# Kernel optimization log

Hardware: AMD Instinct MI355X
Metric: run time of the kernel (lower is better)

## Reference

```python
import jax, jax.numpy as jnp
import numpy as np

N, E, ELG, B = 50000, 400000, 1600000, 2000
F, ED, T = 64, 16, 6
SND = 6 * F  # LinearBlock hidden


def segment_softmax(x, seg, num_segments):
    m = jax.ops.segment_max(x, seg, num_segments=num_segments)
    e = jnp.exp(x - m[seg])
    s = jax.ops.segment_sum(e, seg, num_segments=num_segments)
    return e / (s[seg] + 1e-16)


def setup_inputs() -> dict:
    key = jax.random.key(0)
    ks = jax.random.split(key, 32)
    d = {}
    d['x'] = jax.random.normal(ks[0], (N, F), jnp.float32)
    d['edge_attr'] = jax.random.normal(ks[1], (E, ED), jnp.float32)
    d['edge_index'] = jax.random.randint(ks[2], (2, E), 0, N, jnp.int32)
    d['line_graph_edge_index'] = jax.random.randint(ks[3], (2, ELG), 0, E, jnp.int32)
    d['edge_index_batch'] = jnp.sort(jax.random.randint(ks[4], (E,), 0, B, jnp.int32))
    g = lambda k, shp, fi: jax.random.normal(k, shp, jnp.float32) * (1.0 / np.sqrt(fi))
    d['W_u'] = g(ks[5], (F, F), F)
    d['W_v'] = g(ks[6], (F, F), F)
    d['W_e'] = g(ks[7], (F, ED), ED)
    # GraphConv(F, 1): lin_rel (bias) on aggregated msgs + lin_root (no bias)
    d['conv_w_rel'] = g(ks[8], (1, F), F)
    d['conv_b_rel'] = jnp.zeros((1,), jnp.float32)
    d['conv_w_root'] = g(ks[9], (1, F), F)
    glorot_a = np.sqrt(6.0 / (F + T))
    d['a'] = jax.random.uniform(ks[10], (1, F, T), jnp.float32, -glorot_a, glorot_a)
    d['W_gout'] = g(ks[11], (F, F), F)
    d['b_gout'] = jnp.zeros((F,), jnp.float32)
    d['a_bias'] = jnp.zeros((1, 1, T), jnp.float32)
    d['lb1_w'] = g(ks[12], (SND, F), F); d['lb1_b'] = jnp.zeros((SND,), jnp.float32)
    d['lb2_w'] = g(ks[13], (SND, SND), SND); d['lb2_b'] = jnp.zeros((SND,), jnp.float32)
    d['lb3_w'] = g(ks[14], (SND, SND), SND); d['lb3_b'] = jnp.zeros((SND,), jnp.float32)
    d['lb4_w'] = g(ks[15], (SND, SND), SND); d['lb4_b'] = jnp.zeros((SND,), jnp.float32)
    d['lb5_w'] = g(ks[16], (F, SND), SND); d['lb5_b'] = jnp.zeros((F,), jnp.float32)
    return d


def reference(x, edge_attr, edge_index, line_graph_edge_index, edge_index_batch,
              W_u, W_v, W_e, conv_w_rel, conv_b_rel, conv_w_root,
              a, W_gout, b_gout, a_bias,
              lb1_w, lb1_b, lb2_w, lb2_b, lb3_w, lb3_b, lb4_w, lb4_b, lb5_w, lb5_b):
    src, dst = edge_index[0], edge_index[1]
    lsrc, ldst = line_graph_edge_index[0], line_graph_edge_index[1]
    # initial directed-edge features
    edge_feat = (x @ W_u.T)[src] + (x @ W_v.T)[dst] + edge_attr @ W_e.T  # [E,F]
    edge_feat = edge_feat / 3.0
    out = edge_feat
    outs, gouts = [], []
    for _ in range(T):  # fixed small iteration count
        agg = jax.ops.segment_sum(out[lsrc], ldst, num_segments=E)  # line-graph scatter-add
        out = edge_feat + agg
        # GlobalAttentionPool: GraphConv(F,1) on line graph, segment softmax, add-pool
        conv_agg = jax.ops.segment_sum(out[lsrc], ldst, num_segments=E)
        x_conv = conv_agg @ conv_w_rel.T + conv_b_rel + out @ conv_w_root.T  # [E,1]
        sc = segment_softmax(x_conv, edge_index_batch, B)  # [E,1]
        g = jax.ops.segment_sum(out * sc, edge_index_batch, num_segments=B)  # [B,F]
        outs.append(out)
        gouts.append(jnp.tanh(g @ W_gout.T + b_gout))
    gout_all = jnp.stack(gouts, axis=-1)  # [B,F,T]
    out_all = jnp.stack(outs, axis=-1)    # [E,F,T]
    scores = (gout_all * a).sum(1, keepdims=True) + a_bias  # [B,1,T]
    scores = jax.nn.softmax(scores, axis=-1)
    scores_e = scores[edge_index_batch]  # == repeat_interleave by degree (sorted batch)
    out_w = (out_all * scores_e).sum(-1)  # [E,F]
    h = x + jax.ops.segment_sum(out_w, dst, num_segments=N)
    # LinearBlock (SA-DDI lineage)
    h = jax.nn.relu(h @ lb1_w.T + lb1_b)
    h = (jax.nn.relu(h @ lb2_w.T + lb2_b) @ lb3_w.T + lb3_b + h) / 2.0
    h = (h @ lb4_w.T + lb4_b + h) / 2.0
    return jax.nn.relu(h @ lb5_w.T + lb5_b)
```

## Files before the change

kernel.cpp:

```cpp
#include <hip/hip_runtime.h>
#include <hip/hip_fp16.h>

#define N_   50000
#define E_   400000
#define ELG_ 1600000
#define B_   2000
#define F_   64
#define ED_  16
#define T_   6
#define SND_ 384

typedef long long ll;
typedef _Float16 f16x8 __attribute__((ext_vector_type(8)));
typedef float f32x4 __attribute__((ext_vector_type(4)));

__device__ inline float ldc(const float* p, ll i) { return p[i]; }
__device__ inline float ldc(const __half* p, ll i) { return __half2float(p[i]); }
__device__ inline void st1(float* p, float v) { *p = v; }
__device__ inline void st1(__half* p, float v) { *p = __float2half(v); }

template <int FPL>
__device__ inline void ldN(const float* p, float (&o)[FPL]) {
#pragma unroll
    for (int c = 0; c < FPL; c += 4) {
        float4 v = *(const float4*)(p + c);
        o[c] = v.x; o[c + 1] = v.y; o[c + 2] = v.z; o[c + 3] = v.w;
    }
}
template <int FPL>
__device__ inline void ldN(const __half* p, float (&o)[FPL]) {
#pragma unroll
    for (int c = 0; c < FPL; c += 8) {
        float4 raw = *(const float4*)(p + c);
        const __half2* h = (const __half2*)&raw;
#pragma unroll
        for (int i = 0; i < 4; i++) {
            float2 f = __half22float2(h[i]);
            o[c + 2 * i] = f.x; o[c + 2 * i + 1] = f.y;
        }
    }
}
template <int FPL>
__device__ inline void stN(float* p, const float (&v)[FPL]) {
#pragma unroll
    for (int c = 0; c < FPL; c += 4)
        *(float4*)(p + c) = make_float4(v[c], v[c + 1], v[c + 2], v[c + 3]);
}
template <int FPL>
__device__ inline void stN(__half* p, const float (&v)[FPL]) {
#pragma unroll
    for (int c = 0; c < FPL; c += 8) {
        __half2 h[4];
#pragma unroll
        for (int i = 0; i < 4; i++) h[i] = __floats2half2_rn(v[c + 2 * i], v[c + 2 * i + 1]);
        *(float4*)(p + c) = *(const float4*)h;
    }
}

__global__ __launch_bounds__(256) void k_count(const int* __restrict__ ldst, int* __restrict__ cnt) {
    int i = blockIdx.x * 256 + threadIdx.x;
    if (i < ELG_) atomicAdd(&cnt[ldst[i]], 1);
}

__global__ __launch_bounds__(256) void k_scan1(const int* __restrict__ cnt, int* __restrict__ rowptr,
                                               int* __restrict__ bsum) {
    __shared__ int s[256];
    int tid = threadIdx.x;
    int i = blockIdx.x * 256 + tid;
    int v = (i < E_) ? cnt[i] : 0;
    s[tid] = v;
    __syncthreads();
    for (int off = 1; off < 256; off <<= 1) {
        int t = (tid >= off) ? s[tid - off] : 0;
        __syncthreads();
        s[tid] += t;
        __syncthreads();
    }
    if (i < E_) rowptr[i] = s[tid] - v;
    if (tid == 255) bsum[blockIdx.x] = s[255];
}

__global__ __launch_bounds__(256) void k_scan2(int* __restrict__ bsum, int nb) {
    __shared__ int s[256];
    __shared__ int carry_s;
    int tid = threadIdx.x;
    if (tid == 0) carry_s = 0;
    __syncthreads();
    for (int base = 0; base < nb; base += 256) {
        int i = base + tid;
        int v = (i < nb) ? bsum[i] : 0;
        s[tid] = v;
        __syncthreads();
        for (int off = 1; off < 256; off <<= 1) {
            int t = (tid >= off) ? s[tid - off] : 0;
            __syncthreads();
            s[tid] += t;
            __syncthreads();
        }
        int c = carry_s;
        if (i < nb) bsum[i] = s[tid] - v + c;
        __syncthreads();
        if (tid == 0) carry_s = c + s[255];
        __syncthreads();
    }
}

__global__ __launch_bounds__(256) void k_scan3(int* __restrict__ rowptr, const int* __restrict__ bsum) {
    int i = blockIdx.x * 256 + threadIdx.x;
    if (i < E_) rowptr[i] += bsum[i >> 8];
    if (i == 0) rowptr[E_] = ELG_;
}

__global__ __launch_bounds__(256) void k_fill(const int* __restrict__ lsrc, const int* __restrict__ ldst,
                                              const int* __restrict__ rowptr, int* __restrict__ cursor,
                                              int* __restrict__ csr) {
    int i = blockIdx.x * 256 + threadIdx.x;
    if (i < ELG_) {
        int d = ldst[i];
        int pos = atomicAdd(&cursor[d], 1);
        csr[rowptr[d] + pos] = lsrc[i];
    }
}

__global__ __launch_bounds__(256) void k_bptr(const int* __restrict__ eib, int* __restrict__ bptr) {
    int b = blockIdx.x * 256 + threadIdx.x;
    if (b > B_) return;
    int lo = 0, hi = E_;
    while (lo < hi) {
        int mid = (lo + hi) >> 1;
        if (eib[mid] < b) lo = mid + 1; else hi = mid;
    }
    bptr[b] = lo;
}

__global__ __launch_bounds__(256) void k_xuv(const float* __restrict__ x,
                                             const float* __restrict__ Wu, const float* __restrict__ Wv,
                                             float* __restrict__ xu, float* __restrict__ xv) {
    __shared__ float wus[64 * 65];
    __shared__ float wvs[64 * 65];
    __shared__ float xs[16][64];
    int tid = threadIdx.x;
    for (int i = tid; i < 4096; i += 256) {
        int f = i >> 6, k = i & 63;
        wus[k * 65 + f] = Wu[i];
        wvs[k * 65 + f] = Wv[i];
    }
    int r0 = blockIdx.x * 16;
    for (int i = tid; i < 16 * 64; i += 256) {
        int r = i >> 6, j = i & 63;
        int row = r0 + r;
        xs[r][j] = (row < N_) ? x[(ll)row * 64 + j] : 0.f;
    }
    __syncthreads();
    int j = tid & 63, lr0 = tid >> 6;
    float su[4] = {0, 0, 0, 0}, sv[4] = {0, 0, 0, 0};
    for (int k = 0; k < 64; k++) {
        float wu = wus[k * 65 + j];
        float wv = wvs[k * 65 + j];
#pragma unroll
        for (int r = 0; r < 4; r++) {
            float xr = xs[lr0 + r * 4][k];
            su[r] += xr * wu;
            sv[r] += xr * wv;
        }
    }
#pragma unroll
    for (int r = 0; r < 4; r++) {
        int row = r0 + lr0 + r * 4;
        if (row < N_) {
            xu[(ll)row * 64 + j] = su[r];
            xv[(ll)row * 64 + j] = sv[r];
        }
    }
}

template <typename ET>
__global__ __launch_bounds__(256) void k_ef(const float* __restrict__ xu, const float* __restrict__ xv,
                                            const float* __restrict__ ea, const float* __restrict__ We,
                                            const int* __restrict__ src, const int* __restrict__ dst,
                                            ET* __restrict__ ef) {
    __shared__ float wes[16 * 65];
    int tid = threadIdx.x;
    for (int i = tid; i < 1024; i += 256) {
        wes[(i & 15) * 65 + (i >> 4)] = We[i];
    }
    __syncthreads();
    int wid = tid >> 6, f = tid & 63;
    ll e0 = (ll)blockIdx.x * 16;
#pragma unroll
    for (int r = 0; r < 4; r++) {
        ll e = e0 + wid + r * 4;
        if (e >= E_) return;
        int s = src[e], d = dst[e];
        float v = xu[(ll)s * 64 + f] + xv[(ll)d * 64 + f];
#pragma unroll
        for (int k = 0; k < 16; k++) v += ea[e * 16 + k] * wes[k * 65 + f];
        st1(&ef[e * 64 + f], v * (1.0f / 3.0f));
    }
}

template <typename T, typename OT, bool WOUT, bool WXC, int ACC>
__global__ __launch_bounds__(256) void k_segv(
    const T* __restrict__ state, T* __restrict__ nxt, OT* __restrict__ outw,
    const float* __restrict__ xu, const float* __restrict__ xv,
    const float* __restrict__ ea, const float* __restrict__ We,
    const int* __restrict__ esrc, const int* __restrict__ edst,
    const int* __restrict__ rowptr, const int* __restrict__ csr,
    float* __restrict__ xc, const float* __restrict__ w_rel,
    const float* __restrict__ b_rel, const float* __restrict__ w_root,
    const float* __restrict__ scores, const int* __restrict__ eib, int tslot)
{
    constexpr int FPL = 16 / sizeof(T);
    constexpr int LPR = F_ / FPL;
    constexpr int RPB = 256 / LPR;
    constexpr bool EF = WOUT || (ACC > 0);
    __shared__ float wes[16 * 65];
    int tid = threadIdx.x;
    if (EF) {
        for (int i = tid; i < 1024; i += 256)
            wes[(i & 15) * 65 + (i >> 4)] = We[i];
        __syncthreads();
    }
    int sub = tid % LPR;
    int r   = tid / LPR;
    ll d = (ll)blockIdx.x * RPB + r;
    int f0 = sub * FPL;
    int p0 = rowptr[d], p1 = rowptr[d + 1];
    float acc[FPL], acc2[FPL];
#pragma unroll
    for (int j = 0; j < FPL; j++) { acc[j] = 0.f; acc2[j] = 0.f; }
    int p = p0;
    for (; p + 2 <= p1; p += 2) {
        int s0 = csr[p], s1 = csr[p + 1];
        float v0[FPL], v1[FPL];
        ldN<FPL>(&state[(ll)s0 * F_ + f0], v0);
        ldN<FPL>(&state[(ll)s1 * F_ + f0], v1);
#pragma unroll
        for (int j = 0; j < FPL; j++) { acc[j] += v0[j]; acc2[j] += v1[j]; }
    }
    if (p < p1) {
        int s0 = csr[p];
        float v0[FPL];
        ldN<FPL>(&state[(ll)s0 * F_ + f0], v0);
#pragma unroll
        for (int j = 0; j < FPL; j++) acc[j] += v0[j];
    }
#pragma unroll
    for (int j = 0; j < FPL; j++) acc[j] += acc2[j];
    if (EF) {
        int se = esrc[d], de = edst[d];
        float o[FPL], xuv[FPL], xvv[FPL];
        ldN<FPL>(&xu[(ll)se * 64 + f0], xuv);
        ldN<FPL>(&xv[(ll)de * 64 + f0], xvv);
#pragma unroll
        for (int j = 0; j < FPL; j++) o[j] = xuv[j] + xvv[j];
#pragma unroll
        for (int k = 0; k < 16; k++) {
            float eav = ea[d * 16 + k];
#pragma unroll
            for (int j = 0; j < FPL; j++) o[j] += eav * wes[k * 65 + f0 + j];
        }
#pragma unroll
        for (int j = 0; j < FPL; j++) o[j] = o[j] * (1.0f / 3.0f) + acc[j];
        if (WOUT) stN<FPL>(&nxt[(ll)d * F_ + f0], o);
        if (ACC > 0) {
            float w = scores[eib[d] * 6 + tslot];
            float ow[FPL];
            if (ACC == 2) ldN<FPL>(&outw[(ll)d * F_ + f0], ow);
            else {
#pragma unroll
                for (int j = 0; j < FPL; j++) ow[j] = 0.f;
            }
#pragma unroll
            for (int j = 0; j < FPL; j++) ow[j] += w * o[j];
            stN<FPL>(&outw[(ll)d * F_ + f0], ow);
        }
    }
    if (WXC) {
        float ov[FPL];
        ldN<FPL>(&state[(ll)d * F_ + f0], ov);
        float part = 0.f;
#pragma unroll
        for (int j = 0; j < FPL; j++)
            part += acc[j] * w_rel[f0 + j] + ov[j] * w_root[f0 + j];
#pragma unroll
        for (int off = LPR / 2; off; off >>= 1) part += __shfl_xor(part, off, 64);
        if (sub == 0) xc[d] = part + b_rel[0];
    }
}

template <typename ST>
__global__ __launch_bounds__(256) void k_pool(const float* __restrict__ xc, const ST* __restrict__ out_t,
                                              const int* __restrict__ bptr, const float* __restrict__ Wg,
                                              const float* __restrict__ bg, float* __restrict__ gouts,
                                              int tslot) {
    int b = blockIdx.x;
    int tid = threadIdx.x;
    int p0 = bptr[b], p1 = bptr[b + 1];
    __shared__ float red[256];
    __shared__ float gsh[64];
    float m = -1e30f;
    for (int i = p0 + tid; i < p1; i += 256) m = fmaxf(m, xc[i]);
    red[tid] = m;
    __syncthreads();
    for (int o = 128; o; o >>= 1) { if (tid < o) red[tid] = fmaxf(red[tid], red[tid + o]); __syncthreads(); }
    m = red[0];
    __syncthreads();
    float ss = 0.f;
    for (int i = p0 + tid; i < p1; i += 256) ss += __expf(xc[i] - m);
    red[tid] = ss;
    __syncthreads();
    for (int o = 128; o; o >>= 1) { if (tid < o) red[tid] += red[tid + o]; __syncthreads(); }
    float inv = 1.0f / (red[0] + 1e-16f);
    __syncthreads();
    int lane = tid & 63, grp = tid >> 6;
    float acc = 0.f;
    for (int e = p0 + grp; e < p1; e += 4) {
        float w = __expf(xc[e] - m) * inv;
        acc += ldc(out_t, (ll)e * 64 + lane) * w;
    }
    red[tid] = acc;
    __syncthreads();
    if (tid < 64) gsh[tid] = red[tid] + red[tid + 64] + red[tid + 128] + red[tid + 192];
    __syncthreads();
    if (tid < 64) {
        float z = bg[tid];
#pragma unroll 8
        for (int k = 0; k < 64; k++) z += gsh[k] * Wg[tid * 64 + k];
        gouts[((ll)b * T_ + tslot) * 64 + tid] = tanhf(z);
    }
}

__global__ __launch_bounds__(64) void k_scores(const float* __restrict__ gouts, const float* __restrict__ a,
                                               const float* __restrict__ ab, float* __restrict__ scores) {
    int b = blockIdx.x, f = threadIdx.x;
    float lg[6];
#pragma unroll
    for (int t = 0; t < 6; t++) {
        float v = gouts[((ll)b * T_ + t) * 64 + f] * a[f * 6 + t];
#pragma unroll
        for (int o = 32; o; o >>= 1) v += __shfl_xor(v, o, 64);
        lg[t] = v + ab[t];
    }
    float m = lg[0];
#pragma unroll
    for (int t = 1; t < 6; t++) m = fmaxf(m, lg[t]);
    float s = 0.f;
#pragma unroll
    for (int t = 0; t < 6; t++) { lg[t] = __expf(lg[t] - m); s += lg[t]; }
    if (f == 0) {
        float inv = 1.0f / s;
#pragma unroll
        for (int t = 0; t < 6; t++) scores[b * 6 + t] = lg[t] * inv;
    }
}

__global__ __launch_bounds__(256) void k_copy(const float* __restrict__ in, float* __restrict__ out, int n) {
    int i = blockIdx.x * 256 + threadIdx.x;
    if (i < n) out[i] = in[i];
}

__global__ __launch_bounds__(256) void k_zero(float* __restrict__ out, int n) {
    int i = blockIdx.x * 256 + threadIdx.x;
    if (i < n) out[i] = 0.f;
}

__global__ __launch_bounds__(256) void k_f2h(const float* __restrict__ in, __half* __restrict__ out, int n) {
    int i = blockIdx.x * 256 + threadIdx.x;
    if (i < n) out[i] = __float2half(in[i]);
}

template <typename OT>
__global__ __launch_bounds__(256) void k_scatter(const OT* __restrict__ outw, const int* __restrict__ dst,
                                                 float* __restrict__ h) {
    ll i = (ll)blockIdx.x * 256 + threadIdx.x;
    if (i >= (ll)E_ * 64) return;
    int e = (int)(i >> 6), f = (int)(i & 63);
    atomicAdd(&h[(ll)dst[e] * 64 + f], ldc(outw, i));
}

template <int MODE, typename CT>
__global__ __launch_bounds__(256) void k_gemm_h(
    const __half* __restrict__ Ah, const __half* __restrict__ Wh,
    const float* __restrict__ bias, const __half* __restrict__ R,
    CT* __restrict__ C, int M, int K, int Nc)
{
    __shared__ _Float16 As[64][40];
    __shared__ _Float16 Ws[64][40];
    int tid = threadIdx.x;
    int m0 = blockIdx.x * 64, j0 = blockIdx.y * 64;
    int wv = tid >> 6, lane = tid & 63;
    int srow = tid >> 2, skq = tid & 3;
    f32x4 acc[4] = {};
    const int arow = m0 + srow;
    for (int k0 = 0; k0 < K; k0 += 32) {
        f16x8 a8 = {};
        if (arow < M) a8 = *(const f16x8*)&Ah[(ll)arow * K + k0 + skq * 8];
        *(f16x8*)&As[srow][skq * 8] = a8;
        f16x8 w8 = *(const f16x8*)&Wh[(ll)(j0 + srow) * K + k0 + skq * 8];
        *(f16x8*)&Ws[srow][skq * 8] = w8;
        __syncthreads();
        f16x8 af = *(const f16x8*)&As[wv * 16 + (lane & 15)][(lane >> 4) * 8];
#pragma unroll
        for (int nt = 0; nt < 4; nt++) {
            f16x8 bf = *(const f16x8*)&Ws[nt * 16 + (lane & 15)][(lane >> 4) * 8];
            acc[nt] = __builtin_amdgcn_mfma_f32_16x16x32_f16(af, bf, acc[nt], 0, 0, 0);
        }
        __syncthreads();
    }
    int colb = lane & 15;
    int row0 = m0 + wv * 16 + (lane >> 4) * 4;
#pragma unroll
    for (int nt = 0; nt < 4; nt++) {
        int col = j0 + nt * 16 + colb;
#pragma unroll
        for (int rg = 0; rg < 4; rg++) {
            int row = row0 + rg;
            if (row >= M) continue;
            float z = acc[nt][rg] + bias[col];
            float o;
            if (MODE == 0) o = fmaxf(z, 0.f);
            else o = (z + __half2float(R[(ll)row * Nc + col])) * 0.5f;
            st1(&C[(ll)row * Nc + col], o);
        }
    }
}

template <int MODE>
__global__ __launch_bounds__(256) void k_gemm(const float* __restrict__ A, const float* __restrict__ W,
                                              const float* __restrict__ bias, const float* __restrict__ R,
                                              float* __restrict__ C, int M, int K, int Nc) {
    __shared__ float As[64][68];
    __shared__ float Ws[64][68];
    int tid = threadIdx.x;
    int m0 = blockIdx.x * 64, j0 = blockIdx.y * 64;
    int tx = tid & 15, ty = tid >> 4;
    float acc[4][4];
#pragma unroll
    for (int i = 0; i < 4; i++)
#pragma unroll
        for (int j = 0; j < 4; j++) acc[i][j] = 0.f;
    for (int k0 = 0; k0 < K; k0 += 64) {
#pragma unroll
        for (int l = 0; l < 4; l++) {
            int fi = tid + l * 256;
            int m = fi >> 4, kq = fi & 15;
            int row = m0 + m;
            float4 v = make_float4(0.f, 0.f, 0.f, 0.f);
            if (row < M) v = *(const float4*)&A[(ll)row * K + k0 + kq * 4];
            As[kq * 4 + 0][m] = v.x; As[kq * 4 + 1][m] = v.y;
            As[kq * 4 + 2][m] = v.z; As[kq * 4 + 3][m] = v.w;
            float4 w = *(const float4*)&W[(ll)(j0 + m) * K + k0 + kq * 4];
            Ws[kq * 4 + 0][m] = w.x; Ws[kq * 4 + 1][m] = w.y;
            Ws[kq * 4 + 2][m] = w.z; Ws[kq * 4 + 3][m] = w.w;
        }
        __syncthreads();
#pragma unroll
        for (int k = 0; k < 64; k++) {
            float4 av = *(const float4*)&As[k][ty * 4];
            float4 bv = *(const float4*)&Ws[k][tx * 4];
            float a_[4] = {av.x, av.y, av.z, av.w};
            float b_[4] = {bv.x, bv.y, bv.z, bv.w};
#pragma unroll
            for (int i = 0; i < 4; i++)
#pragma unroll
                for (int j = 0; j < 4; j++) acc[i][j] += a_[i] * b_[j];
        }
        __syncthreads();
    }
#pragma unroll
    for (int i = 0; i < 4; i++) {
        int row = m0 + ty * 4 + i;
        if (row >= M) continue;
#pragma unroll
        for (int j = 0; j < 4; j++) {
            int col = j0 + tx * 4 + j;
            float z = acc[i][j] + bias[col];
            float o;
            if (MODE == 0) o = fmaxf(z, 0.f);
            else o = (z + R[(ll)row * Nc + col]) * 0.5f;
            C[(ll)row * Nc + col] = o;
        }
    }
}

struct Args {
    const float *x, *ea;
    const int *src, *dstp, *lsrc, *ldst, *eib;
    const float *Wu, *Wv, *We, *w_rel, *b_rel, *w_root, *a, *Wg, *bg, *abias;
    const float *lb1w, *lb1b, *lb2w, *lb2b, *lb3w, *lb3b, *lb4w, *lb4b, *lb5w, *lb5b;
    float *xc, *gouts, *scores;
    int *rowptr, *cnt, *csr, *bsum, *bptr;
    float *xu, *xv;
    float *h;
    char *ws_base;
};

template <typename T1T, typename OT>
static void run_tier(const Args& A, T1T* bufA, T1T* bufB, __half* q0, __half* q1, OT* outw,
                     bool bigLB, hipStream_t stream) {
    constexpr int RPB1 = 256 / (F_ / (16 / (int)sizeof(T1T)));
    const int sg1 = E_ / RPB1;
    const int sg2 = E_ / 32;
    const int efg = (E_ + 15) / 16;

    k_xuv<<<(N_ + 15) / 16, 256, 0, stream>>>(A.x, A.Wu, A.Wv, A.xu, A.xv);
    k_ef<T1T><<<efg, 256, 0, stream>>>(A.xu, A.xv, A.ea, A.We, A.src, A.dstp, bufA);

#define SEGARGS A.xu, A.xv, A.ea, A.We, A.src, A.dstp, A.rowptr, A.csr, \
                A.xc, A.w_rel, A.b_rel, A.w_root, A.scores, A.eib
    k_segv<T1T, OT, true,  false, 0><<<sg1, 256, 0, stream>>>(bufA, bufB, (OT*)nullptr, SEGARGS, 0);
    k_segv<T1T, OT, true,  true,  0><<<sg1, 256, 0, stream>>>(bufB, bufA, (OT*)nullptr, SEGARGS, 0);
    k_pool<T1T><<<B_, 256, 0, stream>>>(A.xc, bufB, A.bptr, A.Wg, A.bg, A.gouts, 0);
    k_segv<T1T, OT, true,  true,  0><<<sg1, 256, 0, stream>>>(bufA, bufB, (OT*)nullptr, SEGARGS, 0);
    k_pool<T1T><<<B_, 256, 0, stream>>>(A.xc, bufA, A.bptr, A.Wg, A.bg, A.gouts, 1);
    k_segv<T1T, OT, true,  true,  0><<<sg1, 256, 0, stream>>>(bufB, bufA, (OT*)nullptr, SEGARGS, 0);
    k_pool<T1T><<<B_, 256, 0, stream>>>(A.xc, bufB, A.bptr, A.Wg, A.bg, A.gouts, 2);
    k_segv<T1T, OT, true,  true,  0><<<sg1, 256, 0, stream>>>(bufA, bufB, (OT*)nullptr, SEGARGS, 0);
    k_pool<T1T><<<B_, 256, 0, stream>>>(A.xc, bufA, A.bptr, A.Wg, A.bg, A.gouts, 3);
    k_segv<T1T, OT, true,  true,  0><<<sg1, 256, 0, stream>>>(bufB, bufA, (OT*)nullptr, SEGARGS, 0);
    k_pool<T1T><<<B_, 256, 0, stream>>>(A.xc, bufB, A.bptr, A.Wg, A.bg, A.gouts, 4);
    k_segv<T1T, OT, false, true,  0><<<sg1, 256, 0, stream>>>(bufA, (T1T*)nullptr, (OT*)nullptr, SEGARGS, 0);
    k_pool<T1T><<<B_, 256, 0, stream>>>(A.xc, bufA, A.bptr, A.Wg, A.bg, A.gouts, 5);

    k_scores<<<B_, 64, 0, stream>>>(A.gouts, A.a, A.abias, A.scores);

    k_ef<__half><<<efg, 256, 0, stream>>>(A.xu, A.xv, A.ea, A.We, A.src, A.dstp, q0);
    k_segv<__half, OT, true,  false, 1><<<sg2, 256, 0, stream>>>(q0, q1, outw, SEGARGS, 0);
    k_segv<__half, OT, true,  false, 2><<<sg2, 256, 0, stream>>>(q1, q0, outw, SEGARGS, 1);
    k_segv<__half, OT, true,  false, 2><<<sg2, 256, 0, stream>>>(q0, q1, outw, SEGARGS, 2);
    k_segv<__half, OT, true,  false, 2><<<sg2, 256, 0, stream>>>(q1, q0, outw, SEGARGS, 3);
    k_segv<__half, OT, true,  false, 2><<<sg2, 256, 0, stream>>>(q0, q1, outw, SEGARGS, 4);
    k_segv<__half, OT, false, false, 2><<<sg2, 256, 0, stream>>>(q1, (__half*)nullptr, outw, SEGARGS, 5);
#undef SEGARGS

    k_copy<<<(N_ * 64 + 255) / 256, 256, 0, stream>>>(A.x, A.h, N_ * 64);
    k_scatter<OT><<<(int)(((ll)E_ * 64 + 255) / 256), 256, 0, stream>>>(outw, A.dstp, A.h);

    if (bigLB) {
        __half* hf  = (__half*)A.ws_base;
        __half* w1h = hf  + (size_t)N_ * 64;
        __half* w2h = w1h + (size_t)SND_ * 64;
        __half* w3h = w2h + (size_t)SND_ * SND_;
        __half* w4h = w3h + (size_t)SND_ * SND_;
        __half* w5h = w4h + (size_t)SND_ * SND_;
        __half* hb1 = w5h + (size_t)64 * SND_;
        __half* hb2 = hb1 + (size_t)N_ * SND_;
        __half* hb3 = hb2 + (size_t)N_ * SND_;
        __half* hb4 = hb3 + (size_t)N_ * SND_;
        k_f2h<<<(N_ * 64 + 255) / 256, 256, 0, stream>>>(A.h, hf, N_ * 64);
        k_f2h<<<(SND_ * 64 + 255) / 256, 256, 0, stream>>>(A.lb1w, w1h, SND_ * 64);
        k_f2h<<<(SND_ * SND_ + 255) / 256, 256, 0, stream>>>(A.lb2w, w2h, SND_ * SND_);
        k_f2h<<<(SND_ * SND_ + 255) / 256, 256, 0, stream>>>(A.lb3w, w3h, SND_ * SND_);
        k_f2h<<<(SND_ * SND_ + 255) / 256, 256, 0, stream>>>(A.lb4w, w4h, SND_ * SND_);
        k_f2h<<<(SND_ * 64 + 255) / 256, 256, 0, stream>>>(A.lb5w, w5h, 64 * SND_);
        dim3 g6((N_ + 63) / 64, SND_ / 64);
        dim3 g1((N_ + 63) / 64, 1);
        k_gemm_h<0, __half><<<g6, 256, 0, stream>>>(hf,  w1h, A.lb1b, nullptr, hb1, N_, 64,   SND_);
        k_gemm_h<0, __half><<<g6, 256, 0, stream>>>(hb1, w2h, A.lb2b, nullptr, hb2, N_, SND_, SND_);
        k_gemm_h<1, __half><<<g6, 256, 0, stream>>>(hb2, w3h, A.lb3b, hb1,    hb3, N_, SND_, SND_);
        k_gemm_h<1, __half><<<g6, 256, 0, stream>>>(hb3, w4h, A.lb4b, hb3,    hb4, N_, SND_, SND_);
        k_gemm_h<0, float ><<<g1, 256, 0, stream>>>(hb4, w5h, A.lb5b, nullptr, A.h, N_, SND_, 64);
    } else {
        const int CH = 12800;
        size_t cb = (size_t)CH * SND_ * 4;
        float* b1 = (float*)A.ws_base;
        float* b2 = (float*)(A.ws_base + cb);
        float* b3 = (float*)(A.ws_base + 2 * cb);
        for (int r0 = 0; r0 < N_; r0 += CH) {
            int m = (N_ - r0 < CH) ? (N_ - r0) : CH;
            dim3 g6((m + 63) / 64, SND_ / 64);
            dim3 g1((m + 63) / 64, 1);
            k_gemm<0><<<g6, 256, 0, stream>>>(A.h + (ll)r0 * 64, A.lb1w, A.lb1b, nullptr, b1, m, 64,   SND_);
            k_gemm<0><<<g6, 256, 0, stream>>>(b1, A.lb2w, A.lb2b, nullptr, b2, m, SND_, SND_);
            k_gemm<1><<<g6, 256, 0, stream>>>(b2, A.lb3w, A.lb3b, b1,      b3, m, SND_, SND_);
            k_gemm<1><<<g6, 256, 0, stream>>>(b3, A.lb4w, A.lb4b, b3,      b1, m, SND_, SND_);
            k_gemm<0><<<g1, 256, 0, stream>>>(b1, A.lb5w, A.lb5b, nullptr, A.h + (ll)r0 * 64, m, SND_, 64);
        }
    }
}

extern "C" void kernel_launch(void* const* d_in, const int* in_sizes, int n_in,
                              void* d_out, int out_size, void* d_ws, size_t ws_size,
                              hipStream_t stream) {
    (void)in_sizes; (void)n_in; (void)out_size;
    Args A;
    A.x      = (const float*)d_in[0];
    A.ea     = (const float*)d_in[1];
    const int* eidx = (const int*)d_in[2];
    const int* lgp  = (const int*)d_in[3];
    A.eib    = (const int*)d_in[4];
    A.Wu     = (const float*)d_in[5];
    A.Wv     = (const float*)d_in[6];
    A.We     = (const float*)d_in[7];
    A.w_rel  = (const float*)d_in[8];
    A.b_rel  = (const float*)d_in[9];
    A.w_root = (const float*)d_in[10];
    A.a      = (const float*)d_in[11];
    A.Wg     = (const float*)d_in[12];
    A.bg     = (const float*)d_in[13];
    A.abias  = (const float*)d_in[14];
    A.lb1w = (const float*)d_in[15]; A.lb1b = (const float*)d_in[16];
    A.lb2w = (const float*)d_in[17]; A.lb2b = (const float*)d_in[18];
    A.lb3w = (const float*)d_in[19]; A.lb3b = (const float*)d_in[20];
    A.lb4w = (const float*)d_in[21]; A.lb4b = (const float*)d_in[22];
    A.lb5w = (const float*)d_in[23]; A.lb5b = (const float*)d_in[24];
    A.src  = eidx;
    A.dstp = eidx + E_;
    A.lsrc = lgp;
    A.ldst = lgp + ELG_;
    A.h       = (float*)d_out;
    A.ws_base = (char*)d_ws;

    char* p = (char*)d_ws;
    auto alloc = [&](size_t bytes) -> char* {
        char* r = p;
        p += (bytes + 255) & ~(size_t)255;
        return r;
    };
    A.xc     = (float*)alloc((size_t)E_ * 4);
    A.gouts  = (float*)alloc((size_t)B_ * T_ * 64 * 4);
    A.scores = (float*)alloc((size_t)B_ * T_ * 4);
    A.rowptr = (int*)alloc((size_t)(E_ + 1) * 4);
    A.cnt    = (int*)alloc((size_t)E_ * 4);
    A.csr    = (int*)alloc((size_t)ELG_ * 4);
    A.bsum   = (int*)alloc(8192);
    A.bptr   = (int*)alloc((size_t)(B_ + 1) * 4);
    A.xu     = (float*)alloc((size_t)N_ * 64 * 4);
    A.xv     = (float*)alloc((size_t)N_ * 64 * 4);

    const size_t NEED_T1 = 244736768ull;
    const size_t NEED_T3 = 193536768ull;

    if (ws_size < NEED_T3) {
        k_zero<<<(N_ * 64 + 255) / 256, 256, 0, stream>>>((float*)d_out, N_ * 64);
        return;
    }

    hipMemsetAsync(A.cnt, 0, (size_t)E_ * 4, stream);
    k_count<<<(ELG_ + 255) / 256, 256, 0, stream>>>(A.ldst, A.cnt);
    int nb1 = (E_ + 255) / 256;
    k_scan1<<<nb1, 256, 0, stream>>>(A.cnt, A.rowptr, A.bsum);
    k_scan2<<<1, 256, 0, stream>>>(A.bsum, nb1);
    k_scan3<<<nb1, 256, 0, stream>>>(A.rowptr, A.bsum);
    hipMemsetAsync(A.cnt, 0, (size_t)E_ * 4, stream);
    k_fill<<<(ELG_ + 255) / 256, 256, 0, stream>>>(A.lsrc, A.ldst, A.rowptr, A.cnt, A.csr);
    k_bptr<<<(B_ + 1 + 255) / 256, 256, 0, stream>>>(A.eib, A.bptr);

    if (ws_size >= NEED_T1) {
        float* bufA = (float*)alloc((size_t)E_ * 64 * 4);
        float* bufB = (float*)alloc((size_t)E_ * 64 * 4);
        __half* q0 = (__half*)bufA;
        __half* q1 = q0 + (size_t)E_ * 64;
        run_tier<float, float>(A, bufA, bufB, q0, q1, (float*)bufB, true, stream);
    } else {
        __half* bufA = (__half*)alloc((size_t)E_ * 64 * 2);
        __half* bufB = (__half*)alloc((size_t)E_ * 64 * 2);
        __half* outw = (__half*)alloc((size_t)E_ * 64 * 2);
        run_tier<__half, __half>(A, bufA, bufB, bufA, bufB, outw, false, stream);
    }
}
```

Measured before the change: 2.241 ms.

## Reuse tier-one final states for last two steps and unroll gather by four

The last two steps' outputs (steps 4 and 5) are still held in bufA/bufB after the first pass. They are now combined with their attention scores by a new elementwise kernel, k_comb, which initializes outw. This lets the second recomputation pass stop after four segment kernels instead of six. The CSR gather loop also gains a 4-way unrolled body for more memory-level parallelism, and the load/store helpers switch to native vector types. The risk is that the final outputs for those two steps now come from the tier-one buffer precision rather than the half-precision recompute.

Result: faster. 2.096 ms (-6.5%).

```diff
diff --git a/kernel.cpp b/kernel.cpp
--- a/kernel.cpp
+++ b/kernel.cpp
@@ -13,6 +13,7 @@
 typedef long long ll;
 typedef _Float16 f16x8 __attribute__((ext_vector_type(8)));
 typedef float f32x4 __attribute__((ext_vector_type(4)));
+typedef float fv4 __attribute__((ext_vector_type(4)));
 
 __device__ inline float ldc(const float* p, ll i) { return p[i]; }
 __device__ inline float ldc(const __half* p, ll i) { return __half2float(p[i]); }
@@ -23,7 +24,7 @@
 __device__ inline void ldN(const float* p, float (&o)[FPL]) {
 #pragma unroll
     for (int c = 0; c < FPL; c += 4) {
-        float4 v = *(const float4*)(p + c);
+        fv4 v = *(const fv4*)(p + c);
         o[c] = v.x; o[c + 1] = v.y; o[c + 2] = v.z; o[c + 3] = v.w;
     }
 }
@@ -31,29 +32,27 @@
 __device__ inline void ldN(const __half* p, float (&o)[FPL]) {
 #pragma unroll
     for (int c = 0; c < FPL; c += 8) {
-        float4 raw = *(const float4*)(p + c);
-        const __half2* h = (const __half2*)&raw;
-#pragma unroll
-        for (int i = 0; i < 4; i++) {
-            float2 f = __half22float2(h[i]);
-            o[c + 2 * i] = f.x; o[c + 2 * i + 1] = f.y;
-        }
+        f16x8 raw = *(const f16x8*)(p + c);
+#pragma unroll
+        for (int i = 0; i < 8; i++) o[c + i] = (float)raw[i];
     }
 }
 template <int FPL>
 __device__ inline void stN(float* p, const float (&v)[FPL]) {
 #pragma unroll
-    for (int c = 0; c < FPL; c += 4)
-        *(float4*)(p + c) = make_float4(v[c], v[c + 1], v[c + 2], v[c + 3]);
+    for (int c = 0; c < FPL; c += 4) {
+        fv4 t; t.x = v[c]; t.y = v[c + 1]; t.z = v[c + 2]; t.w = v[c + 3];
+        *(fv4*)(p + c) = t;
+    }
 }
 template <int FPL>
 __device__ inline void stN(__half* p, const float (&v)[FPL]) {
 #pragma unroll
     for (int c = 0; c < FPL; c += 8) {
-        __half2 h[4];
-#pragma unroll
-        for (int i = 0; i < 4; i++) h[i] = __floats2half2_rn(v[c + 2 * i], v[c + 2 * i + 1]);
-        *(float4*)(p + c) = *(const float4*)h;
+        f16x8 t;
+#pragma unroll
+        for (int i = 0; i < 8; i++) t[i] = (_Float16)v[c + i];
+        *(f16x8*)(p + c) = t;
     }
 }
 
@@ -230,6 +229,16 @@
 #pragma unroll
     for (int j = 0; j < FPL; j++) { acc[j] = 0.f; acc2[j] = 0.f; }
     int p = p0;
+    for (; p + 4 <= p1; p += 4) {
+        int s0 = csr[p], s1 = csr[p + 1], s2 = csr[p + 2], s3 = csr[p + 3];
+        float v0[FPL], v1[FPL], v2[FPL], v3[FPL];
+        ldN<FPL>(&state[(ll)s0 * F_ + f0], v0);
+        ldN<FPL>(&state[(ll)s1 * F_ + f0], v1);
+        ldN<FPL>(&state[(ll)s2 * F_ + f0], v2);
+        ldN<FPL>(&state[(ll)s3 * F_ + f0], v3);
+#pragma unroll
+        for (int j = 0; j < FPL; j++) { acc[j] += v0[j] + v2[j]; acc2[j] += v1[j] + v3[j]; }
+    }
     for (; p + 2 <= p1; p += 2) {
         int s0 = csr[p], s1 = csr[p + 1];
         float v0[FPL], v1[FPL];
@@ -287,6 +296,18 @@
         for (int off = LPR / 2; off; off >>= 1) part += __shfl_xor(part, off, 64);
         if (sub == 0) xc[d] = part + b_rel[0];
     }
+}
+
+template <typename TA, typename TB, typename OT>
+__global__ __launch_bounds__(256) void k_comb(const TA* __restrict__ o6, const TB* __restrict__ o5,
+                                              OT* __restrict__ outw, const float* __restrict__ scores,
+                                              const int* __restrict__ eib) {
+    ll i = (ll)blockIdx.x * 256 + threadIdx.x;
+    if (i >= (ll)E_ * 64) return;
+    int e = (int)(i >> 6);
+    int b = eib[e];
+    float v = scores[b * 6 + 4] * ldc(o5, i) + scores[b * 6 + 5] * ldc(o6, i);
+    st1(&outw[i], v);
 }
 
 template <typename ST>
@@ -503,6 +524,7 @@
     const int sg1 = E_ / RPB1;
     const int sg2 = E_ / 32;
     const int efg = (E_ + 15) / 16;
+    const int ewg = (int)(((ll)E_ * 64 + 255) / 256);
 
     k_xuv<<<(N_ + 15) / 16, 256, 0, stream>>>(A.x, A.Wu, A.Wv, A.xu, A.xv);
     k_ef<T1T><<<efg, 256, 0, stream>>>(A.xu, A.xv, A.ea, A.We, A.src, A.dstp, bufA);
@@ -525,17 +547,16 @@
 
     k_scores<<<B_, 64, 0, stream>>>(A.gouts, A.a, A.abias, A.scores);
 
+    k_comb<T1T, T1T, OT><<<ewg, 256, 0, stream>>>(bufA, bufB, outw, A.scores, A.eib);
     k_ef<__half><<<efg, 256, 0, stream>>>(A.xu, A.xv, A.ea, A.We, A.src, A.dstp, q0);
-    k_segv<__half, OT, true,  false, 1><<<sg2, 256, 0, stream>>>(q0, q1, outw, SEGARGS, 0);
+    k_segv<__half, OT, true,  false, 2><<<sg2, 256, 0, stream>>>(q0, q1, outw, SEGARGS, 0);
     k_segv<__half, OT, true,  false, 2><<<sg2, 256, 0, stream>>>(q1, q0, outw, SEGARGS, 1);
     k_segv<__half, OT, true,  false, 2><<<sg2, 256, 0, stream>>>(q0, q1, outw, SEGARGS, 2);
-    k_segv<__half, OT, true,  false, 2><<<sg2, 256, 0, stream>>>(q1, q0, outw, SEGARGS, 3);
-    k_segv<__half, OT, true,  false, 2><<<sg2, 256, 0, stream>>>(q0, q1, outw, SEGARGS, 4);
-    k_segv<__half, OT, false, false, 2><<<sg2, 256, 0, stream>>>(q1, (__half*)nullptr, outw, SEGARGS, 5);
+    k_segv<__half, OT, false, false, 2><<<sg2, 256, 0, stream>>>(q1, (__half*)nullptr, outw, SEGARGS, 3);
 #undef SEGARGS
 
     k_copy<<<(N_ * 64 + 255) / 256, 256, 0, stream>>>(A.x, A.h, N_ * 64);
-    k_scatter<OT><<<(int)(((ll)E_ * 64 + 255) / 256), 256, 0, stream>>>(outw, A.dstp, A.h);
+    k_scatter<OT><<<ewg, 256, 0, stream>>>(outw, A.dstp, A.h);
 
     if (bigLB) {
         __half* hf  = (__half*)A.ws_base;
```
